# Kernel tuning notes

Hardware: AMD Instinct MI355X
Metric: run time of the kernel (lower is better)

## Reference

```python
import jax, jax.numpy as jnp
from jax import lax
import numpy as np

THRESHOLD = 1.25
CURRENT_DECAY = 0.25
VOLTAGE_DECAY = 0.03
TAU_GRAD = 0.03
SCALE_GRAD = 3.0


@jax.custom_vjp
def spike_fn(v):
    # Heaviside spike on membrane voltage (threshold already subtracted)
    return (v >= 0.0).astype(v.dtype)

def _spike_fwd(v):
    return spike_fn(v), v

def _spike_bwd(v, g):
    # slayer-style exponential surrogate gradient around threshold
    surrogate = SCALE_GRAD * jnp.exp(-jnp.abs(v) / TAU_GRAD)
    return (g * surrogate,)

spike_fn.defvjp(_spike_fwd, _spike_bwd)


def cuba_dense(x, v_w, g_w, delay):
    """x: [B, C_in, T] spikes -> [B, C_out, T] spikes.
    Weight-normalized dense synapse + CUBA leaky-integrate-and-fire scan + axonal delay."""
    # weight norm: W = g * v / ||v||_row
    norm = jnp.sqrt(jnp.sum(v_w * v_w, axis=1, keepdims=True))
    W = g_w[:, None] * v_w / norm                       # [O, C]
    z = jnp.einsum('bct,oc->bot', x, W)                 # synaptic current input [B, O, T]
    B, O, T = z.shape
    zT = jnp.transpose(z, (2, 0, 1))                    # [T, B, O]

    def step(carry, zt):
        cur, vol = carry
        cur = cur * (1.0 - CURRENT_DECAY) + zt
        vol = vol * (1.0 - VOLTAGE_DECAY) + cur
        s = spike_fn(vol - THRESHOLD)
        vol = vol * (1.0 - s)                           # reset to zero on spike
        return (cur, vol), s

    init = (jnp.zeros((B, O), z.dtype), jnp.zeros((B, O), z.dtype))
    _, sT = lax.scan(step, init, zT)                    # [T, B, O]
    s = jnp.transpose(sT, (1, 2, 0))                    # [B, O, T]

    # per-neuron integer axonal delay: out[b,n,t] = s[b,n,t-d_n]
    t_idx = jnp.arange(T)[None, :] - delay[:, None]     # [O, T]
    valid = (t_idx >= 0)
    gathered = s[:, jnp.arange(O)[:, None], jnp.clip(t_idx, 0, T - 1)]
    return jnp.where(valid[None, :, :], gathered, jnp.zeros((), s.dtype))


def setup_inputs() -> dict:
    key = jax.random.key(0)
    ks = jax.random.split(key, 10)
    B, C, T = 32, 34 * 34 * 2, 300
    spike = (jax.random.uniform(ks[0], (B, C, T)) < 0.1).astype(jnp.float32)
    v1 = jax.random.normal(ks[1], (512, C), jnp.float32) * 0.1
    g1 = jax.random.uniform(ks[2], (512,), jnp.float32) + 0.5
    v2 = jax.random.normal(ks[3], (512, 512), jnp.float32) * 0.1
    g2 = jax.random.uniform(ks[4], (512,), jnp.float32) + 0.5
    v3 = jax.random.normal(ks[5], (10, 512), jnp.float32) * 0.1
    g3 = jax.random.uniform(ks[6], (10,), jnp.float32) + 0.5
    d1 = jax.random.randint(ks[7], (512,), 0, 8, jnp.int32)
    d2 = jax.random.randint(ks[8], (512,), 0, 8, jnp.int32)
    d3 = jax.random.randint(ks[9], (10,), 0, 8, jnp.int32)
    return {"spike": spike, "v1": v1, "g1": g1, "v2": v2, "g2": g2,
            "v3": v3, "g3": g3, "d1": d1, "d2": d2, "d3": d3}


def reference(spike, v1, g1, v2, g2, v3, g3, d1, d2, d3):
    s1 = cuba_dense(spike, v1, g1, d1)
    s2 = cuba_dense(s1, v2, g2, d2)
    s3 = cuba_dense(s2, v3, g3, d3)
    counts = jnp.stack([jnp.mean(s1), jnp.mean(s2), jnp.mean(s3)]).reshape(1, -1)
    return s3, counts
```

## Files before the change

### kernel.cpp

```cpp
#include <hip/hip_runtime.h>

#define B_   32
#define T_   300
#define C1_  2312
#define O1_  512
#define O2_  512
#define O3_  10
#define M_   (B_*T_)
#define KSPLIT_ 1152


__global__ void calc_f(const float* __restrict__ v, const float* __restrict__ g,
                       double* __restrict__ f, int O, int C) {
    int o = blockIdx.x;
    const float* row = v + (size_t)o * C;
    double s = 0.0;
    for (int c = threadIdx.x; c < C; c += blockDim.x) {
        double x = (double)row[c];
        s += x * x;
    }
    for (int off = 32; off; off >>= 1) s += __shfl_down(s, off);
    __shared__ double wsum[4];
    int lane = threadIdx.x & 63, wv = threadIdx.x >> 6;
    if (lane == 0) wsum[wv] = s;
    __syncthreads();
    if (threadIdx.x == 0) {
        double tot = 0.0;
        for (int i = 0; i < (int)(blockDim.x >> 6); ++i) tot += wsum[i];
        f[o] = (double)g[o] / sqrt(tot);
    }
}

__global__ void transpose_scale(const float* __restrict__ v, const double* __restrict__ f,
                                double* __restrict__ wt, int O, int C, int ldo) {
    __shared__ double tile[32][33];
    int c0 = blockIdx.x * 32, o0 = blockIdx.y * 32;
    int tx = threadIdx.x, ty = threadIdx.y;
    for (int k = 0; k < 4; ++k) {
        int o = o0 + ty + k * 8, c = c0 + tx;
        double val = 0.0;
        if (o < O && c < C) val = (double)v[(size_t)o * C + c] * f[o];
        tile[ty + k * 8][tx] = val;
    }
    __syncthreads();
    for (int k = 0; k < 4; ++k) {
        int c = c0 + ty + k * 8, o = o0 + tx;
        if (c < C && o < O) wt[(size_t)c * ldo + o] = tile[tx][ty + k * 8];
    }
}

__global__ void build_bits(const float* __restrict__ X, unsigned* __restrict__ bits) {
    size_t idx = (size_t)blockIdx.x * 256 + threadIdx.x;
    if (idx >= (size_t)B_ * C1_ * 10) return;
    int t32 = (int)(idx % 10);
    size_t bc = idx / 10;
    const float* src = X + bc * T_ + t32 * 32;
    int nq = (t32 == 9) ? 3 : 8;
    unsigned m = 0;
    for (int q = 0; q < nq; ++q) {
        float4 v = *(const float4*)(src + q * 4);
        if (v.x != 0.f) m |= 1u << (q * 4 + 0);
        if (v.y != 0.f) m |= 1u << (q * 4 + 1);
        if (v.z != 0.f) m |= 1u << (q * 4 + 2);
        if (v.w != 0.f) m |= 1u << (q * 4 + 3);
    }
    bits[idx] = m;
}

__global__ __launch_bounds__(256) void gemm1(const unsigned* __restrict__ Xbits,
                                             const double* __restrict__ Wt,
                                             double* __restrict__ Z) {
    __shared__ double Ws[16][256];
    int n = blockIdx.x;
    int xg = n & 7;
    int combo = xg & 3;
    int khalf = combo & 1;
    int o0 = (combo >> 1) * 256;
    int i = n >> 3;
    int tb = i % 10;
    int b = (i / 10) * 2 + (xg >> 2);
    int cbeg = khalf ? KSPLIT_ : 0;
    const int NT = khalf ? 73 : 72;
    int tid = threadIdx.x;
    int lane = tid & 63;
    int w8s = __builtin_amdgcn_readfirstlane((tid >> 6) << 3);
    double acc[8][4];
#pragma unroll
    for (int tj = 0; tj < 8; ++tj)
#pragma unroll
        for (int i2 = 0; i2 < 4; ++i2) acc[tj][i2] = 0.0;
    const unsigned* xbp = Xbits + (size_t)b * C1_ * 10 + tb;

    double2 wreg[8];
    unsigned mk[16], mkn[16];

    auto load_w = [&](int c0) {
#pragma unroll
        for (int h = 0; h < 8; ++h) {
            int idx = h * 256 + tid;
            int r = idx >> 7, od = (idx & 127) * 2;
            int c = c0 + r;
            double2 val; val.x = 0.0; val.y = 0.0;
            if (c < C1_) val = *(const double2*)(Wt + (size_t)c * O1_ + o0 + od);
            wreg[h] = val;
        }
    };
    auto load_m = [&](unsigned* dst, int c0) {
#pragma unroll
        for (int k = 0; k < 16; ++k) {
            int c = c0 + k;
            dst[k] = (c < C1_) ? xbp[(size_t)c * 10] : 0u;
        }
    };
    auto store_w = [&]() {
#pragma unroll
        for (int h = 0; h < 8; ++h) {
            int idx = h * 256 + tid;
            int r = idx >> 7, od = (idx & 127) * 2;
            *(double2*)(&Ws[r][od]) = wreg[h];
        }
    };

    load_w(cbeg);
    load_m(mk, cbeg);
    for (int tile = 0; tile < NT; ++tile) {
        store_w();
        __syncthreads();
        if (tile + 1 < NT) {
            int cn = cbeg + (tile + 1) * 16;
            load_w(cn);
            load_m(mkn, cn);
        }
#pragma unroll
        for (int k = 0; k < 16; ++k) {
            unsigned smk = (unsigned)__builtin_amdgcn_readfirstlane((int)mk[k]);
            unsigned soct = (smk >> w8s) & 0xffu;
            if (soct) {
                double wf[4];
#pragma unroll
                for (int i2 = 0; i2 < 4; ++i2) wf[i2] = Ws[k][lane + 64 * i2];
#pragma unroll
                for (int tj = 0; tj < 8; ++tj) {
                    if (soct & (1u << tj)) {
#pragma unroll
                        for (int i2 = 0; i2 < 4; ++i2) acc[tj][i2] += wf[i2];
                    }
                }
            }
        }
#pragma unroll
        for (int k = 0; k < 16; ++k) mk[k] = mkn[k];
        __syncthreads();
    }
#pragma unroll
    for (int tj = 0; tj < 8; ++tj) {
        int t = tb * 32 + w8s + tj;
        if (t < T_) {
            double* dst = Z + ((size_t)b * T_ + t) * O1_ + o0;
#pragma unroll
            for (int i2 = 0; i2 < 4; ++i2)
                atomicAdd(&dst[lane + 64 * i2], acc[tj][i2]);
        }
    }
}

__global__ __launch_bounds__(256) void gemm2(const float* __restrict__ A,
                                             const double* __restrict__ Wt,
                                             double* __restrict__ Z) {
    __shared__ double Ws[16][128];
    __shared__ double As[64][17];
    int m0 = blockIdx.x * 64;
    int o0 = blockIdx.y * 128;
    int tid = threadIdx.x;
    int to = tid & 15, tm = tid >> 4;
    double acc[8][4];
#pragma unroll
    for (int i = 0; i < 8; ++i)
#pragma unroll
        for (int j = 0; j < 4; ++j) acc[i][j] = 0.0;
    for (int c0 = 0; c0 < 512; c0 += 16) {
        {
            int m = tid >> 2, ch = (tid & 3) * 4;
            float4 v = *(const float4*)(A + (size_t)(m0 + m) * 512 + c0 + ch);
            As[m][ch + 0] = (double)v.x; As[m][ch + 1] = (double)v.y;
            As[m][ch + 2] = (double)v.z; As[m][ch + 3] = (double)v.w;
        }
#pragma unroll
        for (int h = 0; h < 4; ++h) {
            int idx = h * 512 + tid * 2;
            int i = idx >> 7, o = idx & 127;
            *(double2*)(&Ws[i][o]) = *(const double2*)(Wt + (size_t)(c0 + i) * 512 + o0 + o);
        }
        __syncthreads();
#pragma unroll
        for (int k = 0; k < 16; ++k) {
            double wf[8], xf[4];
#pragma unroll
            for (int i = 0; i < 8; ++i) wf[i] = Ws[k][to + 16 * i];
#pragma unroll
            for (int j = 0; j < 4; ++j) xf[j] = As[tm * 4 + j][k];
#pragma unroll
            for (int i = 0; i < 8; ++i)
#pragma unroll
                for (int j = 0; j < 4; ++j) acc[i][j] = fma(wf[i], xf[j], acc[i][j]);
        }
        __syncthreads();
    }
#pragma unroll
    for (int j = 0; j < 4; ++j) {
        double* dst = Z + (size_t)(m0 + tm * 4 + j) * 512 + o0;
#pragma unroll
        for (int i = 0; i < 8; ++i) dst[to + 16 * i] = acc[i][j];
    }
}

__global__ void gemm3(const float* __restrict__ A,
                      const double* __restrict__ Wt,
                      double* __restrict__ Z) {
    __shared__ double w[512 * 16];
    for (int e = threadIdx.x; e < 4096; e += 256)
        ((double2*)w)[e] = ((const double2*)Wt)[e];
    __syncthreads();
    int m = blockIdx.x * 256 + threadIdx.x;
    if (m >= M_) return;
    double acc[O3_];
#pragma unroll
    for (int o = 0; o < O3_; ++o) acc[o] = 0.0;
    const float4* Ar = (const float4*)(A + (size_t)m * 512);
    for (int cq = 0; cq < 128; ++cq) {
        float4 a = Ar[cq];
        float av[4] = {a.x, a.y, a.z, a.w};
#pragma unroll
        for (int u = 0; u < 4; ++u)
#pragma unroll
            for (int o = 0; o < O3_; ++o) acc[o] += (double)av[u] * w[(cq * 4 + u) * 16 + o];
    }
    double* dst = Z + (size_t)m * 16;
#pragma unroll
    for (int o = 0; o < O3_; ++o) dst[o] = acc[o];
}

__global__ void scan12(const double* __restrict__ Zin,
                       const int* __restrict__ delay,
                       float* __restrict__ Sout,
                       float* __restrict__ sumOut) {
    int blk = blockIdx.x;
    int o = (blk & 7) * 64 + threadIdx.x;
    int b = blk >> 3;
    const double* z = Zin + (size_t)b * T_ * O1_ + o;
    float* s = Sout + (size_t)b * T_ * O1_ + o;
    int d = delay[o];
    for (int t = 0; t < d; ++t) s[(size_t)t * O1_] = 0.f;
    double cur = 0.0, vol = 0.0;
    float cnt = 0.f;
    for (int t8 = 0; t8 < 296; t8 += 8) {
        double zb[8];
#pragma unroll
        for (int u = 0; u < 8; ++u) zb[u] = z[(size_t)(t8 + u) * O1_];
#pragma unroll
        for (int u = 0; u < 8; ++u) {
            int t = t8 + u;
            cur = cur * 0.75 + zb[u];
            vol = vol * 0.97 + cur;
            float sp = (vol >= 1.25) ? 1.f : 0.f;
            if (sp > 0.f) vol = 0.0;
            int tw = t + d;
            if (tw < T_) { s[(size_t)tw * O1_] = sp; cnt += sp; }
        }
    }
    {
        double zb[4];
#pragma unroll
        for (int u = 0; u < 4; ++u) zb[u] = z[(size_t)(296 + u) * O1_];
#pragma unroll
        for (int u = 0; u < 4; ++u) {
            int t = 296 + u;
            cur = cur * 0.75 + zb[u];
            vol = vol * 0.97 + cur;
            float sp = (vol >= 1.25) ? 1.f : 0.f;
            if (sp > 0.f) vol = 0.0;
            int tw = t + d;
            if (tw < T_) { s[(size_t)tw * O1_] = sp; cnt += sp; }
        }
    }
    for (int off = 32; off; off >>= 1) cnt += __shfl_down(cnt, off);
    if (threadIdx.x == 0) atomicAdd(sumOut, cnt);
}

__global__ void scan3(const double* __restrict__ Z3,
                      const int* __restrict__ d3,
                      float* __restrict__ out,
                      float* __restrict__ sumOut) {
    __shared__ double zt[T_ * 16];
    int b = blockIdx.x;
    const double2* src = (const double2*)(Z3 + (size_t)b * T_ * 16);
    for (int e = threadIdx.x; e < T_ * 8; e += 64)
        ((double2*)zt)[e] = src[e];
    __syncthreads();
    int o = threadIdx.x;
    if (o < O3_) {
        int d = d3[o];
        float* dst = out + (size_t)b * O3_ * T_ + (size_t)o * T_;
        for (int t = 0; t < d; ++t) dst[t] = 0.f;
        double cur = 0.0, vol = 0.0;
        float cnt = 0.f;
        for (int t = 0; t < T_; ++t) {
            cur = cur * 0.75 + zt[t * 16 + o];
            vol = vol * 0.97 + cur;
            float sp = (vol >= 1.25) ? 1.f : 0.f;
            if (sp > 0.f) vol = 0.0;
            int tw = t + d;
            if (tw < T_) { dst[tw] = sp; cnt += sp; }
        }
        atomicAdd(sumOut, cnt);
    }
}

__global__ void finalize(const float* __restrict__ sums, float* __restrict__ out) {
    if (threadIdx.x == 0) {
        out[0] = (float)((double)sums[0] / (double)(B_ * O1_ * T_));
        out[1] = (float)((double)sums[1] / (double)(B_ * O2_ * T_));
        out[2] = (float)((double)sums[2] / (double)(B_ * O3_ * T_));
    }
}

extern "C" void kernel_launch(void* const* d_in, const int* in_sizes, int n_in,
                              void* d_out, int out_size, void* d_ws, size_t ws_size,
                              hipStream_t stream) {
    const float* spike = (const float*)d_in[0];
    const float* v1 = (const float*)d_in[1];
    const float* g1 = (const float*)d_in[2];
    const float* v2 = (const float*)d_in[3];
    const float* g2 = (const float*)d_in[4];
    const float* v3 = (const float*)d_in[5];
    const float* g3 = (const float*)d_in[6];
    const int* d1 = (const int*)d_in[7];
    const int* d2 = (const int*)d_in[8];
    const int* d3 = (const int*)d_in[9];
    float* out = (float*)d_out;

    double* dw = (double*)d_ws;
    size_t off = 0;
    double* f1  = dw + off; off += 512;
    double* f2  = dw + off; off += 512;
    double* f3  = dw + off; off += 16;
    double* Wt1 = dw + off; off += (size_t)C1_ * O1_;
    double* Wt2 = dw + off; off += 512 * 512;
    double* Wt3 = dw + off; off += 512 * 16;
    double* zA  = dw + off; off += (size_t)M_ * 512;
    double* z3b = dw + off; off += (size_t)M_ * 16;
    float* fw = (float*)(dw + off);
    float* sB    = fw;
    float* sums  = fw + (size_t)M_ * 512;
    unsigned* Xbits = (unsigned*)(fw + (size_t)M_ * 512 + 4);
    (void)ws_size; (void)out_size; (void)in_sizes; (void)n_in;

    hipMemsetAsync(sums, 0, 4 * sizeof(float), stream);
    hipMemsetAsync(zA, 0, (size_t)M_ * 512 * sizeof(double), stream);

    build_bits<<<(B_ * C1_ * 10 + 255) / 256, 256, 0, stream>>>(spike, Xbits);

    calc_f<<<512, 256, 0, stream>>>(v1, g1, f1, O1_, C1_);
    calc_f<<<512, 256, 0, stream>>>(v2, g2, f2, O2_, O1_);
    calc_f<<<O3_, 256, 0, stream>>>(v3, g3, f3, O3_, O2_);

    transpose_scale<<<dim3((C1_ + 31) / 32, 16), dim3(32, 8), 0, stream>>>(v1, f1, Wt1, O1_, C1_, O1_);
    transpose_scale<<<dim3(16, 16), dim3(32, 8), 0, stream>>>(v2, f2, Wt2, O2_, O1_, O2_);
    transpose_scale<<<dim3(16, 1), dim3(32, 8), 0, stream>>>(v3, f3, Wt3, O3_, O2_, 16);

    gemm1<<<1280, 256, 0, stream>>>(Xbits, Wt1, zA);
    scan12<<<256, 64, 0, stream>>>(zA, d1, sB, sums + 0);
    gemm2<<<dim3(M_ / 64, 4), 256, 0, stream>>>(sB, Wt2, zA);
    scan12<<<256, 64, 0, stream>>>(zA, d2, sB, sums + 1);
    gemm3<<<(M_ + 255) / 256, 256, 0, stream>>>(sB, Wt3, z3b);
    scan3<<<B_, 64, 0, stream>>>(z3b, d3, out, sums + 2);
    finalize<<<1, 64, 0, stream>>>(sums, out + (size_t)B_ * O3_ * T_);
}
```

Before: 846.4 us.

## Replace dense layer-2 GEMM with spike-bitmask sparse accumulation and widen gemm1 blocks

The layer-1 scan now also writes a per-neuron 32-step spike bitmask, and a new gemm2s consumes it with the same skip-zero accumulation scheme as gemm1, in place of the dense FP64 FMA GEMM on float spikes. gemm1 moves to 512-thread blocks that cover two batches per block, and it shares the weight tile across 8 waves. Each lane now holds one mask word that is broadcast with readlane, instead of every lane keeping 16 words in registers. This is meant to avoid dense multiply work on sparse spikes and to halve the weight-tile loads per output. The cost is extra bitmask stores in the scan and more register pressure from the larger blocks.

Result: no change. 854.3 us (+0.9%).

```diff
diff --git a/kernel.cpp b/kernel.cpp
--- a/kernel.cpp
+++ b/kernel.cpp
@@ -67,23 +67,24 @@
     bits[idx] = m;
 }
 
-__global__ __launch_bounds__(256) void gemm1(const unsigned* __restrict__ Xbits,
-                                             const double* __restrict__ Wt,
-                                             double* __restrict__ Z) {
+__global__ __launch_bounds__(512, 4) void gemm1(const unsigned* __restrict__ Xbits,
+                                                const double* __restrict__ Wt,
+                                                double* __restrict__ Z) {
     __shared__ double Ws[16][256];
     int n = blockIdx.x;
-    int xg = n & 7;
-    int combo = xg & 3;
+    int combo = n & 3;
     int khalf = combo & 1;
     int o0 = (combo >> 1) * 256;
-    int i = n >> 3;
+    int i = n >> 2;
     int tb = i % 10;
-    int b = (i / 10) * 2 + (xg >> 2);
+    int bpair = i / 10;
+    int tid = threadIdx.x;
+    int w = tid >> 6;
+    int lane = tid & 63;
+    int b = bpair * 2 + (w >> 2);
+    int w8s = __builtin_amdgcn_readfirstlane((w & 3) << 3);
     int cbeg = khalf ? KSPLIT_ : 0;
     const int NT = khalf ? 73 : 72;
-    int tid = threadIdx.x;
-    int lane = tid & 63;
-    int w8s = __builtin_amdgcn_readfirstlane((tid >> 6) << 3);
     double acc[8][4];
 #pragma unroll
     for (int tj = 0; tj < 8; ++tj)
@@ -91,13 +92,13 @@
         for (int i2 = 0; i2 < 4; ++i2) acc[tj][i2] = 0.0;
     const unsigned* xbp = Xbits + (size_t)b * C1_ * 10 + tb;
 
-    double2 wreg[8];
-    unsigned mk[16], mkn[16];
+    double2 wreg[4];
+    unsigned mval, mvaln = 0u;
 
     auto load_w = [&](int c0) {
 #pragma unroll
-        for (int h = 0; h < 8; ++h) {
-            int idx = h * 256 + tid;
+        for (int h = 0; h < 4; ++h) {
+            int idx = h * 512 + tid;
             int r = idx >> 7, od = (idx & 127) * 2;
             int c = c0 + r;
             double2 val; val.x = 0.0; val.y = 0.0;
@@ -105,35 +106,32 @@
             wreg[h] = val;
         }
     };
-    auto load_m = [&](unsigned* dst, int c0) {
-#pragma unroll
-        for (int k = 0; k < 16; ++k) {
-            int c = c0 + k;
-            dst[k] = (c < C1_) ? xbp[(size_t)c * 10] : 0u;
-        }
+    auto load_m = [&](int c0) -> unsigned {
+        int c = c0 + lane;
+        return (lane < 16 && c < C1_) ? xbp[(size_t)c * 10] : 0u;
     };
     auto store_w = [&]() {
 #pragma unroll
-        for (int h = 0; h < 8; ++h) {
-            int idx = h * 256 + tid;
+        for (int h = 0; h < 4; ++h) {
+            int idx = h * 512 + tid;
             int r = idx >> 7, od = (idx & 127) * 2;
             *(double2*)(&Ws[r][od]) = wreg[h];
         }
     };
 
     load_w(cbeg);
-    load_m(mk, cbeg);
+    mval = load_m(cbeg);
     for (int tile = 0; tile < NT; ++tile) {
         store_w();
         __syncthreads();
         if (tile + 1 < NT) {
             int cn = cbeg + (tile + 1) * 16;
             load_w(cn);
-            load_m(mkn, cn);
+            mvaln = load_m(cn);
         }
 #pragma unroll
         for (int k = 0; k < 16; ++k) {
-            unsigned smk = (unsigned)__builtin_amdgcn_readfirstlane((int)mk[k]);
+            unsigned smk = (unsigned)__builtin_amdgcn_readlane((int)mval, k);
             unsigned soct = (smk >> w8s) & 0xffu;
             if (soct) {
                 double wf[4];
@@ -148,8 +146,7 @@
                 }
             }
         }
-#pragma unroll
-        for (int k = 0; k < 16; ++k) mk[k] = mkn[k];
+        mval = mvaln;
         __syncthreads();
     }
 #pragma unroll
@@ -164,53 +161,92 @@
     }
 }
 
-__global__ __launch_bounds__(256) void gemm2(const float* __restrict__ A,
-                                             const double* __restrict__ Wt,
-                                             double* __restrict__ Z) {
-    __shared__ double Ws[16][128];
-    __shared__ double As[64][17];
-    int m0 = blockIdx.x * 64;
-    int o0 = blockIdx.y * 128;
+__global__ __launch_bounds__(512, 4) void gemm2s(const unsigned* __restrict__ Sbits,
+                                                 const double* __restrict__ Wt,
+                                                 double* __restrict__ Z) {
+    __shared__ double Ws[16][256];
+    int n = blockIdx.x;
+    int ohalf = n & 1;
+    int o0 = ohalf * 256;
+    int i = n >> 1;
+    int twin = i % 5;
+    int b = i / 5;
     int tid = threadIdx.x;
-    int to = tid & 15, tm = tid >> 4;
+    int w = tid >> 6;
+    int lane = tid & 63;
+    int w8s = __builtin_amdgcn_readfirstlane((w & 3) << 3);
+    int word = twin * 2 + (w >> 2);
     double acc[8][4];
 #pragma unroll
-    for (int i = 0; i < 8; ++i)
-#pragma unroll
-        for (int j = 0; j < 4; ++j) acc[i][j] = 0.0;
-    for (int c0 = 0; c0 < 512; c0 += 16) {
-        {
-            int m = tid >> 2, ch = (tid & 3) * 4;
-            float4 v = *(const float4*)(A + (size_t)(m0 + m) * 512 + c0 + ch);
-            As[m][ch + 0] = (double)v.x; As[m][ch + 1] = (double)v.y;
-            As[m][ch + 2] = (double)v.z; As[m][ch + 3] = (double)v.w;
-        }
+    for (int tj = 0; tj < 8; ++tj)
+#pragma unroll
+        for (int i2 = 0; i2 < 4; ++i2) acc[tj][i2] = 0.0;
+    const unsigned* xbp = Sbits + (size_t)b * O1_ * 10 + word;
+
+    double2 wreg[4];
+    unsigned mval, mvaln = 0u;
+
+    auto load_w = [&](int c0) {
 #pragma unroll
         for (int h = 0; h < 4; ++h) {
-            int idx = h * 512 + tid * 2;
-            int i = idx >> 7, o = idx & 127;
-            *(double2*)(&Ws[i][o]) = *(const double2*)(Wt + (size_t)(c0 + i) * 512 + o0 + o);
-        }
+            int idx = h * 512 + tid;
+            int r = idx >> 7, od = (idx & 127) * 2;
+            int c = c0 + r;
+            wreg[h] = *(const double2*)(Wt + (size_t)c * O2_ + o0 + od);
+        }
+    };
+    auto load_m = [&](int c0) -> unsigned {
+        int c = c0 + lane;
+        return (lane < 16) ? xbp[(size_t)c * 10] : 0u;
+    };
+    auto store_w = [&]() {
+#pragma unroll
+        for (int h = 0; h < 4; ++h) {
+            int idx = h * 512 + tid;
+            int r = idx >> 7, od = (idx & 127) * 2;
+            *(double2*)(&Ws[r][od]) = wreg[h];
+        }
+    };
+
+    load_w(0);
+    mval = load_m(0);
+    for (int tile = 0; tile < 32; ++tile) {
+        store_w();
         __syncthreads();
+        if (tile + 1 < 32) {
+            int cn = (tile + 1) * 16;
+            load_w(cn);
+            mvaln = load_m(cn);
+        }
 #pragma unroll
         for (int k = 0; k < 16; ++k) {
-            double wf[8], xf[4];
-#pragma unroll
-            for (int i = 0; i < 8; ++i) wf[i] = Ws[k][to + 16 * i];
-#pragma unroll
-            for (int j = 0; j < 4; ++j) xf[j] = As[tm * 4 + j][k];
-#pragma unroll
-            for (int i = 0; i < 8; ++i)
-#pragma unroll
-                for (int j = 0; j < 4; ++j) acc[i][j] = fma(wf[i], xf[j], acc[i][j]);
-        }
+            unsigned smk = (unsigned)__builtin_amdgcn_readlane((int)mval, k);
+            unsigned soct = (smk >> w8s) & 0xffu;
+            if (soct) {
+                double wf[4];
+#pragma unroll
+                for (int i2 = 0; i2 < 4; ++i2) wf[i2] = Ws[k][lane + 64 * i2];
+#pragma unroll
+                for (int tj = 0; tj < 8; ++tj) {
+                    if (soct & (1u << tj)) {
+#pragma unroll
+                        for (int i2 = 0; i2 < 4; ++i2) acc[tj][i2] += wf[i2];
+                    }
+                }
+            }
+        }
+        mval = mvaln;
         __syncthreads();
     }
 #pragma unroll
-    for (int j = 0; j < 4; ++j) {
-        double* dst = Z + (size_t)(m0 + tm * 4 + j) * 512 + o0;
-#pragma unroll
-        for (int i = 0; i < 8; ++i) dst[to + 16 * i] = acc[i][j];
+    for (int tj = 0; tj < 8; ++tj) {
+        int t = twin * 64 + w * 8 + tj;
+        if (t < T_) {
+            double* dst = Z + ((size_t)b * T_ + t) * O2_ + o0;
+#pragma unroll
+            for (int i2 = 0; i2 < 4; ++i2)
+                dst[lane + 64 * i2] = acc[tj][i2];
+        }
     }
 }
 
@@ -243,16 +279,19 @@
 __global__ void scan12(const double* __restrict__ Zin,
                        const int* __restrict__ delay,
                        float* __restrict__ Sout,
+                       unsigned* __restrict__ bitsOut,
                        float* __restrict__ sumOut) {
     int blk = blockIdx.x;
     int o = (blk & 7) * 64 + threadIdx.x;
     int b = blk >> 3;
     const double* z = Zin + (size_t)b * T_ * O1_ + o;
     float* s = Sout + (size_t)b * T_ * O1_ + o;
+    unsigned* bp = bitsOut + ((size_t)b * O1_ + o) * 10;
     int d = delay[o];
     for (int t = 0; t < d; ++t) s[(size_t)t * O1_] = 0.f;
     double cur = 0.0, vol = 0.0;
     float cnt = 0.f;
+    unsigned bw = 0u;
     for (int t8 = 0; t8 < 296; t8 += 8) {
         double zb[8];
 #pragma unroll
@@ -265,7 +304,11 @@
             float sp = (vol >= 1.25) ? 1.f : 0.f;
             if (sp > 0.f) vol = 0.0;
             int tw = t + d;
-            if (tw < T_) { s[(size_t)tw * O1_] = sp; cnt += sp; }
+            if (tw < T_) {
+                s[(size_t)tw * O1_] = sp; cnt += sp;
+                if (sp > 0.f) bw |= 1u << (tw & 31);
+                if ((tw & 31) == 31) { bp[tw >> 5] = bw; bw = 0u; }
+            }
         }
     }
     {
@@ -280,9 +323,14 @@
             float sp = (vol >= 1.25) ? 1.f : 0.f;
             if (sp > 0.f) vol = 0.0;
             int tw = t + d;
-            if (tw < T_) { s[(size_t)tw * O1_] = sp; cnt += sp; }
-        }
-    }
+            if (tw < T_) {
+                s[(size_t)tw * O1_] = sp; cnt += sp;
+                if (sp > 0.f) bw |= 1u << (tw & 31);
+                if ((tw & 31) == 31) { bp[tw >> 5] = bw; bw = 0u; }
+            }
+        }
+    }
+    bp[9] = bw;
     for (int off = 32; off; off >>= 1) cnt += __shfl_down(cnt, off);
     if (threadIdx.x == 0) atomicAdd(sumOut, cnt);
 }
@@ -353,6 +401,7 @@
     float* sB    = fw;
     float* sums  = fw + (size_t)M_ * 512;
     unsigned* Xbits = (unsigned*)(fw + (size_t)M_ * 512 + 4);
+    unsigned* bits2 = Xbits + (size_t)B_ * C1_ * 10;
     (void)ws_size; (void)out_size; (void)in_sizes; (void)n_in;
 
     hipMemsetAsync(sums, 0, 4 * sizeof(float), stream);
@@ -368,10 +417,10 @@
     transpose_scale<<<dim3(16, 16), dim3(32, 8), 0, stream>>>(v2, f2, Wt2, O2_, O1_, O2_);
     transpose_scale<<<dim3(16, 1), dim3(32, 8), 0, stream>>>(v3, f3, Wt3, O3_, O2_, 16);
 
-    gemm1<<<1280, 256, 0, stream>>>(Xbits, Wt1, zA);
-    scan12<<<256, 64, 0, stream>>>(zA, d1, sB, sums + 0);
-    gemm2<<<dim3(M_ / 64, 4), 256, 0, stream>>>(sB, Wt2, zA);
-    scan12<<<256, 64, 0, stream>>>(zA, d2, sB, sums + 1);
+    gemm1<<<640, 512, 0, stream>>>(Xbits, Wt1, zA);
+    scan12<<<256, 64, 0, stream>>>(zA, d1, sB, bits2, sums + 0);
+    gemm2s<<<320, 512, 0, stream>>>(bits2, Wt2, zA);
+    scan12<<<256, 64, 0, stream>>>(zA, d2, sB, bits2, sums + 1);
     gemm3<<<(M_ + 255) / 256, 256, 0, stream>>>(sB, Wt3, z3b);
     scan3<<<B_, 64, 0, stream>>>(z3b, d3, out, sums + 2);
     finalize<<<1, 64, 0, stream>>>(sums, out + (size_t)B_ * O3_ * T_);
```
